# Kernel tuning notes

Measured on AMD Instinct MI355X. Metric: run time of the kernel, lower is better.

The kernel has to match this reference:

```python
import jax, jax.numpy as jnp
import numpy as np

KS = 5
NF = 64
B, H, W = 2, 160, 160


def _conv1x1(x, w, b):
    # x: (B,Ci,H,W), w: (Co,Ci)
    return jnp.einsum('oi,bihw->bohw', w, x) + b[None, :, None, None]


def _conv2x2(x, w, b, dil):
    # x: (B,1,Hp,Wp), w: (64,1,2,2); VALID conv with dilation dil
    y = jax.lax.conv_general_dilated(x, w, (1, 1), 'VALID',
                                     rhs_dilation=(dil, dil),
                                     dimension_numbers=('NCHW', 'OIHW', 'NCHW'))
    return y + b[None, :, None, None]


def _conv_s(x, w, b):
    # conv1 module, mode 's': gather taps (0,0),(1,1),(1,2),(2,1) of each 3x3 patch,
    # then (1,4) conv == linear combo of 4 shifted images.
    h = x.shape[2] - 2
    wd = x.shape[3] - 2
    x0 = x[:, 0]
    taps = jnp.stack([x0[:, 0:h, 0:wd],
                      x0[:, 1:h + 1, 1:wd + 1],
                      x0[:, 1:h + 1, 2:wd + 2],
                      x0[:, 2:h + 2, 1:wd + 1]], axis=1)  # (B,4,h,wd)
    return jnp.einsum('ok,bkhw->bohw', w.reshape(NF, 4), taps) + b[None, :, None, None]


def _construct(c, dense_ps):
    # relu then dense 1x1-conv chain with channel concat, final 1x1 -> 4 channels
    x = jax.nn.relu(c)
    for (wt, bs) in dense_ps[:-1]:
        feat = jax.nn.relu(_conv1x1(x, wt, bs))
        x = jnp.concatenate([x, feat], axis=1)
    wt, bs = dense_ps[-1]
    return _conv1x1(x, wt, bs)


def _ag(x, sigx, sigy, theta, sigr):
    # x: (B,ks,ks,HW); params: (B,HW). Per-pixel anisotropic bilateral kernel.
    ks = x.shape[1]
    r = jnp.arange(ks, dtype=x.dtype) - ks // 2
    sq = (r[:, None] ** 2 + r[None, :] ** 2)[None, :, :, None]  # (1,ks,ks,1)
    sx = sigx[:, None, None, :]
    sy = sigy[:, None, None, :]
    th = theta[:, None, None, :]
    sr = sigr[:, None, None, :]
    spatial = jnp.exp(-sq / (2.0 * sr ** 2))
    disx = jnp.abs(x[:, ks // 2:ks // 2 + 1] - x)       # center row
    disy = jnp.abs(x[:, :, ks // 2:ks // 2 + 1] - x)    # center col
    a = sx * disx
    bb = sy * disy
    color = jnp.exp(-0.5 * (a ** 2 - 2.0 * th * a * bb + bb ** 2))
    kern = spatial * color
    kern = kern / jnp.sum(kern, axis=(1, 2), keepdims=True)
    return jnp.sum(kern * x, axis=(1, 2))  # (B,HW)


def _forward(x_in, conv1x_w, conv1x_b, conv1c_w, conv1c_b, conv1cs_w, conv1cs_b,
             w2, b2, w3, b3, w4, b4, w5, b5, w6, b6):
    dense_ps = [(w2, b2), (w3, b3), (w4, b4), (w5, b5), (w6, b6)]

    def fk(x, mod):
        if mod == 's':
            c = _conv_s(x, conv1cs_w, conv1cs_b)
        elif mod == 'c':
            c = _conv2x2(x, conv1c_w, conv1c_b, 2)
        else:
            c = _conv2x2(x, conv1x_w, conv1x_b, 1)
        return _construct(c, dense_ps)

    def mode_ens(x, p, mod):
        pad = lambda z: jnp.pad(z, ((0, 0), (0, 0), (0, p), (0, p)), mode='reflect')
        r0 = fk(pad(x), mod)
        r2 = jnp.rot90(fk(pad(jnp.rot90(x, 2, (2, 3))), mod), 2, (2, 3))
        r1 = jnp.rot90(fk(pad(jnp.rot90(x, 1, (2, 3))), mod), 3, (2, 3))
        r3 = jnp.rot90(fk(pad(jnp.rot90(x, 3, (2, 3))), mod), 1, (2, 3))
        return (r0 + r2) / 2.0, (r1 + r3) / 2.0

    e1x, e2x = mode_ens(x_in, 1, 'x')
    e1s, e2s = mode_ens(x_in, 2, 's')
    e1c, e2c = mode_ens(x_in, 2, 'c')
    par = (e1x + e2x + e1s + e2s + e1c + e2c) / 6.0  # (B,4,H,W)

    b, c, h, w = x_in.shape
    sigx = jnp.clip(jax.nn.sigmoid(par[:, 0]).reshape(b, -1) + 1e-6, 0.0, 1.0)
    sigy = jnp.clip(jax.nn.sigmoid(par[:, 1]).reshape(b, -1) + 1e-6, 0.0, 1.0)
    theta = jnp.clip(jnp.tanh(par[:, 2]).reshape(b, -1), -1.0, 1.0)
    sigr = jnp.clip(jnp.tanh(par[:, 3]).reshape(b, -1) + 1e-6, -1.0, 1.0)

    ph = KS // 2
    xt = jnp.pad(x_in, ((0, 0), (0, 0), (ph, ph), (ph, ph)))  # zero pad
    # unfold -> (B, KS, KS, H*W)
    patches = jnp.stack([jnp.stack([xt[:, 0, i:i + h, j:j + w].reshape(b, -1)
                                    for j in range(KS)], axis=1)
                         for i in range(KS)], axis=1)
    outs = _ag(patches, sigx * 20.0, sigy * 20.0, theta, sigr * 10.0 + 10.0).reshape(b, c, h, w)
    return outs, sigx, sigy, theta, sigr


def setup_inputs() -> dict:
    key = jax.random.key(0)
    k = jax.random.split(key, 10)
    def kn(kk, shape, fan_in):
        return jax.random.normal(kk, shape, jnp.float32) * np.float32(np.sqrt(2.0 / fan_in))
    zb = lambda n: jnp.zeros((n,), jnp.float32)
    return {
        'x_in': jax.random.normal(k[0], (B, 1, H, W), jnp.float32),
        'conv1x_w': kn(k[1], (NF, 1, 2, 2), 4), 'conv1x_b': zb(NF),
        'conv1c_w': kn(k[2], (NF, 1, 2, 2), 4), 'conv1c_b': zb(NF),
        'conv1cs_w': kn(k[3], (NF, 1, 1, 4), 4), 'conv1cs_b': zb(NF),
        'w2': kn(k[4], (NF, NF), NF), 'b2': zb(NF),
        'w3': kn(k[5], (NF, 2 * NF), 2 * NF), 'b3': zb(NF),
        'w4': kn(k[6], (NF, 3 * NF), 3 * NF), 'b4': zb(NF),
        'w5': kn(k[7], (NF, 4 * NF), 4 * NF), 'b5': zb(NF),
        'w6': kn(k[8], (4, 5 * NF), 5 * NF), 'b6': zb(4),
    }


def reference(x_in, conv1x_w, conv1x_b, conv1c_w, conv1c_b, conv1cs_w, conv1cs_b,
              w2, b2, w3, b3, w4, b4, w5, b5, w6, b6):
    return _forward(x_in, conv1x_w, conv1x_b, conv1c_w, conv1c_b, conv1cs_w, conv1cs_b,
                    w2, b2, w3, b3, w4, b4, w5, b5, w6, b6)
```

## Files before the change

kernel.cpp:

```cpp
#include <hip/hip_runtime.h>
#include <hip/hip_bf16.h>
#include <math.h>
#include <string.h>


#define NN   160
#define NPIX 25600

typedef __attribute__((ext_vector_type(4))) float float4v;
typedef __attribute__((ext_vector_type(8))) unsigned short ushort8;
typedef __attribute__((ext_vector_type(2))) unsigned int uint2v;
typedef __attribute__((ext_vector_type(4))) unsigned int uint4v;
typedef __attribute__((ext_vector_type(8))) __bf16 bf16x8;

#define PINV(v) asm volatile("" : "+v"(v))

__device__ __forceinline__ int refp(int a) { return (a <= NN - 1) ? a : (2 * (NN - 1) - a); }

__device__ __forceinline__ unsigned int pk2(float lo, float hi) {
    float2 f; f.x = lo; f.y = hi;
    __hip_bfloat162 h = __float22bfloat162_rn(f);
    unsigned int u;
    memcpy(&u, &h, 4);
    return u;
}
__device__ __forceinline__ uint4v cvt8(const float* __restrict__ p) {
    const float4v f0 = *(const float4v*)p;
    const float4v f1 = *(const float4v*)(p + 4);
    uint4v u;
    u[0] = pk2(f0[0], f0[1]); u[1] = pk2(f0[2], f0[3]);
    u[2] = pk2(f1[0], f1[1]); u[3] = pk2(f1[2], f1[3]);
    return u;
}

template <int NCH>
__device__ __forceinline__ void dense_layer(const uint4v (&A)[NCH], float4v biasv,
                                            unsigned short* Xs, int w, int lo16, int lq) {
    const int K = NCH * 32;
#pragma unroll
    for (int pp = 0; pp < 2; ++pp) {
        const int px0 = (pp * 2) * 16 + lo16;
        const int px1 = (pp * 2 + 1) * 16 + lo16;
        float4v acc0 = biasv, acc1 = biasv;
#pragma unroll
        for (int s = 0; s < NCH; ++s) {
            const int c8 = s * 4 + lq;
            const bf16x8 bf0 = __builtin_bit_cast(bf16x8, *(const ushort8*)&Xs[c8 * 512 + px0 * 8]);
            const bf16x8 bf1 = __builtin_bit_cast(bf16x8, *(const ushort8*)&Xs[c8 * 512 + px1 * 8]);
            const bf16x8 af  = __builtin_bit_cast(bf16x8, A[s]);
            acc0 = __builtin_amdgcn_mfma_f32_16x16x32_bf16(af, bf0, acc0, 0, 0, 0);
            acc1 = __builtin_amdgcn_mfma_f32_16x16x32_bf16(af, bf1, acc1, 0, 0, 0);
        }
        const int cb = K + w * 16 + lq * 4;
        uint2v o0, o1;
        o0[0] = pk2(fmaxf(acc0[0], 0.0f), fmaxf(acc0[1], 0.0f));
        o0[1] = pk2(fmaxf(acc0[2], 0.0f), fmaxf(acc0[3], 0.0f));
        o1[0] = pk2(fmaxf(acc1[0], 0.0f), fmaxf(acc1[1], 0.0f));
        o1[1] = pk2(fmaxf(acc1[2], 0.0f), fmaxf(acc1[3], 0.0f));
        *(uint2v*)&Xs[(cb >> 3) * 512 + px0 * 8 + (cb & 7)] = o0;
        *(uint2v*)&Xs[(cb >> 3) * 512 + px1 * 8 + (cb & 7)] = o1;
    }
    __syncthreads();
}

__global__ __launch_bounds__(256, 3) void bnet_mlp_kernel(
    const float* __restrict__ x,
    const float* __restrict__ wx, const float* __restrict__ bx,
    const float* __restrict__ wcs, const float* __restrict__ bcs,
    const float* __restrict__ wc, const float* __restrict__ bc,
    const float* __restrict__ w2, const float* __restrict__ b2,
    const float* __restrict__ w3, const float* __restrict__ b3,
    const float* __restrict__ w4, const float* __restrict__ b4,
    const float* __restrict__ w5, const float* __restrict__ b5,
    const float* __restrict__ w6,
    float* __restrict__ par)
{
    __shared__ unsigned short Xs[20480];

    const int t = threadIdx.x;
    const int lane = t & 63;
    const int lo16 = lane & 15;
    const int lq = lane >> 4;
    const int w = __builtin_amdgcn_readfirstlane(t >> 6);

    const int arow = w * 16 + lo16;
    uint4v a2[2], a3[4], a4[6], a5[8], a6[3];
#pragma unroll
    for (int s = 0; s < 2; ++s) a2[s] = cvt8(&w2[arow * 64 + s * 32 + lq * 8]);
#pragma unroll
    for (int s = 0; s < 4; ++s) a3[s] = cvt8(&w3[arow * 128 + s * 32 + lq * 8]);
#pragma unroll
    for (int s = 0; s < 6; ++s) a4[s] = cvt8(&w4[arow * 192 + s * 32 + lq * 8]);
#pragma unroll
    for (int s = 0; s < 8; ++s) a5[s] = cvt8(&w5[arow * 256 + s * 32 + lq * 8]);
#pragma unroll
    for (int c = 0; c < 3; ++c) {
        const int ch = (3 * w + c) * 32;
        if (ch < 320 && lo16 < 4) {
            a6[c] = cvt8(&w6[lo16 * 320 + ch + lq * 8]);
        } else {
            uint4v z = {0u, 0u, 0u, 0u};
            a6[c] = z;
        }
    }
    float4v b2v = *(const float4v*)&b2[w * 16 + lq * 4];
    float4v b3v = *(const float4v*)&b3[w * 16 + lq * 4];
    float4v b4v = *(const float4v*)&b4[w * 16 + lq * 4];
    float4v b5v = *(const float4v*)&b5[w * 16 + lq * 4];

#pragma unroll
    for (int s = 0; s < 2; ++s) PINV(a2[s]);
#pragma unroll
    for (int s = 0; s < 4; ++s) PINV(a3[s]);
#pragma unroll
    for (int s = 0; s < 6; ++s) PINV(a4[s]);
#pragma unroll
    for (int s = 0; s < 8; ++s) PINV(a5[s]);
#pragma unroll
    for (int c = 0; c < 3; ++c) PINV(a6[c]);
    PINV(b2v); PINV(b3v); PINV(b4v); PINV(b5v);

    const int bid = blockIdx.x;
    const int nit = 12 + (bid < 384 ? 1 : 0);
    const int g0  = (bid < 384) ? bid * 13 : bid * 12 + 384;

    for (int it = 0; it < nit; ++it) {
        const int g = g0 + it;
        const int v = g % 12;
        const int tb = g / 12;
        const int tile = tb >> 1;
        const int b = tb & 1;
        const int mode = v >> 2;
        const int k = v & 3;

        const float* xb = x + b * NPIX;
        const float* w1 = (mode == 0) ? wx : (mode == 1) ? wcs : wc;
        const float* b1 = (mode == 0) ? bx : (mode == 1) ? bcs : bc;
        int DY[4], DX[4];
        if (mode == 0)      { DY[0]=0; DY[1]=0; DY[2]=1; DY[3]=1;  DX[0]=0; DX[1]=1; DX[2]=0; DX[3]=1; }
        else if (mode == 1) { DY[0]=0; DY[1]=1; DY[2]=1; DY[3]=2;  DX[0]=0; DX[1]=1; DX[2]=2; DX[3]=1; }
        else                { DY[0]=0; DY[1]=0; DY[2]=2; DY[3]=2;  DX[0]=0; DX[1]=2; DX[2]=0; DX[3]=2; }

        const int pix = tile * 64 + lane;
        const int pi = pix / NN;
        const int pj = pix - pi * NN;

        __syncthreads();

        float s4[4];
#pragma unroll
        for (int tt = 0; tt < 4; ++tt) {
            const int dy = DY[tt], dx = DX[tt];
            int r, c;
            if (k == 0)      { r = refp(pi + dy); c = refp(pj + dx); }
            else if (k == 1) { r = refp(pi + dx); c = (pj >= dy) ? (pj - dy) : (dy - pj); }
            else if (k == 2) { r = (pi >= dy) ? (pi - dy) : (dy - pi);
                               c = (pj >= dx) ? (pj - dx) : (dx - pj); }
            else             { r = (pi >= dx) ? (pi - dx) : (dx - pi); c = refp(pj + dy); }
            s4[tt] = xb[r * NN + c];
        }
        float co[16];
#pragma unroll
        for (int oo = 0; oo < 16; ++oo) {
            const int o = w * 16 + oo;
            float cacc = b1[o];
#pragma unroll
            for (int tt = 0; tt < 4; ++tt) cacc = fmaf(w1[o * 4 + tt], s4[tt], cacc);
            co[oo] = fmaxf(cacc, 0.0f);
        }
        uint4v pka, pkb;
#pragma unroll
        for (int q = 0; q < 4; ++q) {
            pka[q] = pk2(co[2 * q], co[2 * q + 1]);
            pkb[q] = pk2(co[8 + 2 * q], co[9 + 2 * q]);
        }
        *(uint4v*)&Xs[(w * 2) * 512 + lane * 8]     = pka;
        *(uint4v*)&Xs[(w * 2 + 1) * 512 + lane * 8] = pkb;
        __syncthreads();

        dense_layer<2>(a2, b2v, Xs, w, lo16, lq);
        dense_layer<4>(a3, b3v, Xs, w, lo16, lq);
        dense_layer<6>(a4, b4v, Xs, w, lo16, lq);
        dense_layer<8>(a5, b5v, Xs, w, lo16, lq);

#pragma unroll
        for (int pt = 0; pt < 4; ++pt) {
            float4v acc6 = {0.f, 0.f, 0.f, 0.f};
            const int px = pt * 16 + lo16;
#pragma unroll
            for (int c = 0; c < 3; ++c) {
                int chb = (3 * w + c) * 32;
                chb = (chb < 288) ? chb : 288;
                const int c8 = (chb >> 3) + lq;
                const bf16x8 bf = __builtin_bit_cast(
                    bf16x8, *(const ushort8*)&Xs[c8 * 512 + px * 8]);
                const bf16x8 af = __builtin_bit_cast(bf16x8, a6[c]);
                acc6 = __builtin_amdgcn_mfma_f32_16x16x32_bf16(af, bf, acc6, 0, 0, 0);
            }
            if (lq == 0) {
                const int pixg = tile * 64 + pt * 16 + lo16;
#pragma unroll
                for (int r = 0; r < 4; ++r)
                    atomicAdd(&par[(r * 2 + b) * NPIX + pixg], acc6[r]);
            }
        }
    }
}

__global__ __launch_bounds__(128) void bnet_bilateral_kernel(
    const float* __restrict__ x, const float* __restrict__ b6,
    float* __restrict__ out)
{
    const int tid = blockIdx.x * 128 + threadIdx.x;
    const int b = tid / NPIX;
    const int pix = tid - b * NPIX;
    const int pi = pix / NN;
    const int pj = pix - pi * NN;

    float* par = out + 2 * NPIX;
    const float inv12 = 1.0f / 12.0f;
    const float p0 = par[(0 + b) * NPIX + pix] * inv12 + b6[0];
    const float p1 = par[(2 + b) * NPIX + pix] * inv12 + b6[1];
    const float p2 = par[(4 + b) * NPIX + pix] * inv12 + b6[2];
    const float p3 = par[(6 + b) * NPIX + pix] * inv12 + b6[3];

    float sigx = 1.0f / (1.0f + __expf(-p0)) + 1e-6f;
    sigx = fminf(fmaxf(sigx, 0.0f), 1.0f);
    float sigy = 1.0f / (1.0f + __expf(-p1)) + 1e-6f;
    sigy = fminf(fmaxf(sigy, 0.0f), 1.0f);
    float t2 = __expf(2.0f * fminf(fmaxf(p2, -15.0f), 15.0f));
    float th = (t2 - 1.0f) / (t2 + 1.0f);
    th = fminf(fmaxf(th, -1.0f), 1.0f);
    float t3 = __expf(2.0f * fminf(fmaxf(p3, -15.0f), 15.0f));
    float sigr = (t3 - 1.0f) / (t3 + 1.0f) + 1e-6f;
    sigr = fminf(fmaxf(sigr, -1.0f), 1.0f);

    par[(0 + b) * NPIX + pix] = sigx;
    par[(2 + b) * NPIX + pix] = sigy;
    par[(4 + b) * NPIX + pix] = th;
    par[(6 + b) * NPIX + pix] = sigr;

    const float sx = sigx * 20.0f;
    const float sy = sigy * 20.0f;
    const float sr = sigr * 10.0f + 10.0f;

    const float* xb = x + b * NPIX;
    float patch[5][5];
#pragma unroll
    for (int ky = 0; ky < 5; ++ky) {
#pragma unroll
        for (int kx = 0; kx < 5; ++kx) {
            const int r = pi + ky - 2, c = pj + kx - 2;
            patch[ky][kx] = (r >= 0 && r < NN && c >= 0 && c < NN) ? xb[r * NN + c] : 0.0f;
        }
    }

    const float inv2sr2 = 1.0f / (2.0f * sr * sr);
    float num = 0.0f, den = 0.0f;
#pragma unroll
    for (int ky = 0; ky < 5; ++ky) {
#pragma unroll
        for (int kx = 0; kx < 5; ++kx) {
            const float v = patch[ky][kx];
            const float dxv = fabsf(patch[2][kx] - v);
            const float dyv = fabsf(patch[ky][2] - v);
            const float a = sx * dxv;
            const float bb = sy * dyv;
            const float sq = (float)((ky - 2) * (ky - 2) + (kx - 2) * (kx - 2));
            const float kern = __expf(-sq * inv2sr2 - 0.5f * (a * a - 2.0f * th * a * bb + bb * bb));
            den += kern;
            num = fmaf(kern, v, num);
        }
    }
    out[tid] = num / den;
}

extern "C" void kernel_launch(void* const* d_in, const int* in_sizes, int n_in,
                              void* d_out, int out_size, void* d_ws, size_t ws_size,
                              hipStream_t stream) {
    const float* x   = (const float*)d_in[0];
    const float* wx  = (const float*)d_in[1];
    const float* bx  = (const float*)d_in[2];
    const float* wc  = (const float*)d_in[3];
    const float* bc  = (const float*)d_in[4];
    const float* wcs = (const float*)d_in[5];
    const float* bcs = (const float*)d_in[6];
    const float* w2  = (const float*)d_in[7];
    const float* b2  = (const float*)d_in[8];
    const float* w3  = (const float*)d_in[9];
    const float* b3  = (const float*)d_in[10];
    const float* w4  = (const float*)d_in[11];
    const float* b4  = (const float*)d_in[12];
    const float* w5  = (const float*)d_in[13];
    const float* b5  = (const float*)d_in[14];
    const float* w6  = (const float*)d_in[15];
    const float* b6  = (const float*)d_in[16];
    float* out = (float*)d_out;

    (void)hipMemsetAsync(out + 2 * NPIX, 0, 8 * NPIX * sizeof(float), stream);

    hipLaunchKernelGGL(bnet_mlp_kernel, dim3(768), dim3(256), 0, stream,
                       x, wx, bx, wcs, bcs, wc, bc,
                       w2, b2, w3, b3, w4, b4, w5, b5, w6,
                       out + 2 * NPIX);

    hipLaunchKernelGGL(bnet_bilateral_kernel, dim3(400), dim3(128), 0, stream,
                       x, b6, out);
}
```

Before: 185.1 us.

## Retile dense MFMA layers as 2x2 output-channel by pixel blocks per wave

After: 212.7 us. 14.9% more time.

```diff
diff --git a/kernel.cpp b/kernel.cpp
--- a/kernel.cpp
+++ b/kernel.cpp
@@ -34,36 +34,48 @@
 }
 
 template <int NCH>
-__device__ __forceinline__ void dense_layer(const uint4v (&A)[NCH], float4v biasv,
-                                            unsigned short* Xs, int w, int lo16, int lq) {
+__device__ __forceinline__ void dense_layer(const uint4v (&A0)[NCH], const uint4v (&A1)[NCH],
+                                            const float* __restrict__ bias,
+                                            unsigned short* Xs,
+                                            int oh, int ph, int lo16, int lq) {
     const int K = NCH * 32;
-#pragma unroll
-    for (int pp = 0; pp < 2; ++pp) {
-        const int px0 = (pp * 2) * 16 + lo16;
-        const int px1 = (pp * 2 + 1) * 16 + lo16;
-        float4v acc0 = biasv, acc1 = biasv;
-#pragma unroll
-        for (int s = 0; s < NCH; ++s) {
-            const int c8 = s * 4 + lq;
-            const bf16x8 bf0 = __builtin_bit_cast(bf16x8, *(const ushort8*)&Xs[c8 * 512 + px0 * 8]);
-            const bf16x8 bf1 = __builtin_bit_cast(bf16x8, *(const ushort8*)&Xs[c8 * 512 + px1 * 8]);
-            const bf16x8 af  = __builtin_bit_cast(bf16x8, A[s]);
-            acc0 = __builtin_amdgcn_mfma_f32_16x16x32_bf16(af, bf0, acc0, 0, 0, 0);
-            acc1 = __builtin_amdgcn_mfma_f32_16x16x32_bf16(af, bf1, acc1, 0, 0, 0);
-        }
-        const int cb = K + w * 16 + lq * 4;
-        uint2v o0, o1;
-        o0[0] = pk2(fmaxf(acc0[0], 0.0f), fmaxf(acc0[1], 0.0f));
-        o0[1] = pk2(fmaxf(acc0[2], 0.0f), fmaxf(acc0[3], 0.0f));
-        o1[0] = pk2(fmaxf(acc1[0], 0.0f), fmaxf(acc1[1], 0.0f));
-        o1[1] = pk2(fmaxf(acc1[2], 0.0f), fmaxf(acc1[3], 0.0f));
-        *(uint2v*)&Xs[(cb >> 3) * 512 + px0 * 8 + (cb & 7)] = o0;
-        *(uint2v*)&Xs[(cb >> 3) * 512 + px1 * 8 + (cb & 7)] = o1;
-    }
+    const int px0 = (ph * 2) * 16 + lo16;
+    const int px1 = (ph * 2 + 1) * 16 + lo16;
+    const float4v bv0 = *(const float4v*)&bias[(oh * 2) * 16 + lq * 4];
+    const float4v bv1 = *(const float4v*)&bias[(oh * 2 + 1) * 16 + lq * 4];
+
+    float4v acc00 = {0.f,0.f,0.f,0.f}, acc01 = acc00, acc10 = acc00, acc11 = acc00;
+#pragma unroll
+    for (int s = 0; s < NCH; ++s) {
+        const int c8 = s * 4 + lq;
+        const bf16x8 bf0 = __builtin_bit_cast(bf16x8, *(const ushort8*)&Xs[c8 * 512 + px0 * 8]);
+        const bf16x8 bf1 = __builtin_bit_cast(bf16x8, *(const ushort8*)&Xs[c8 * 512 + px1 * 8]);
+        const bf16x8 af0 = __builtin_bit_cast(bf16x8, A0[s]);
+        const bf16x8 af1 = __builtin_bit_cast(bf16x8, A1[s]);
+        acc00 = __builtin_amdgcn_mfma_f32_16x16x32_bf16(af0, bf0, acc00, 0, 0, 0);
+        acc01 = __builtin_amdgcn_mfma_f32_16x16x32_bf16(af0, bf1, acc01, 0, 0, 0);
+        acc10 = __builtin_amdgcn_mfma_f32_16x16x32_bf16(af1, bf0, acc10, 0, 0, 0);
+        acc11 = __builtin_amdgcn_mfma_f32_16x16x32_bf16(af1, bf1, acc11, 0, 0, 0);
+    }
+    const int cb0 = K + (oh * 2) * 16 + lq * 4;
+    const int cb1 = K + (oh * 2 + 1) * 16 + lq * 4;
+    uint2v o00, o01, o10, o11;
+    o00[0] = pk2(fmaxf(acc00[0] + bv0[0], 0.0f), fmaxf(acc00[1] + bv0[1], 0.0f));
+    o00[1] = pk2(fmaxf(acc00[2] + bv0[2], 0.0f), fmaxf(acc00[3] + bv0[3], 0.0f));
+    o01[0] = pk2(fmaxf(acc01[0] + bv0[0], 0.0f), fmaxf(acc01[1] + bv0[1], 0.0f));
+    o01[1] = pk2(fmaxf(acc01[2] + bv0[2], 0.0f), fmaxf(acc01[3] + bv0[3], 0.0f));
+    o10[0] = pk2(fmaxf(acc10[0] + bv1[0], 0.0f), fmaxf(acc10[1] + bv1[1], 0.0f));
+    o10[1] = pk2(fmaxf(acc10[2] + bv1[2], 0.0f), fmaxf(acc10[3] + bv1[3], 0.0f));
+    o11[0] = pk2(fmaxf(acc11[0] + bv1[0], 0.0f), fmaxf(acc11[1] + bv1[1], 0.0f));
+    o11[1] = pk2(fmaxf(acc11[2] + bv1[2], 0.0f), fmaxf(acc11[3] + bv1[3], 0.0f));
+    *(uint2v*)&Xs[(cb0 >> 3) * 512 + px0 * 8 + (cb0 & 7)] = o00;
+    *(uint2v*)&Xs[(cb0 >> 3) * 512 + px1 * 8 + (cb0 & 7)] = o01;
+    *(uint2v*)&Xs[(cb1 >> 3) * 512 + px0 * 8 + (cb1 & 7)] = o10;
+    *(uint2v*)&Xs[(cb1 >> 3) * 512 + px1 * 8 + (cb1 & 7)] = o11;
     __syncthreads();
 }
 
-__global__ __launch_bounds__(256, 3) void bnet_mlp_kernel(
+__global__ __launch_bounds__(256, 2) void bnet_mlp_kernel(
     const float* __restrict__ x,
     const float* __restrict__ wx, const float* __restrict__ bx,
     const float* __restrict__ wcs, const float* __restrict__ bcs,
@@ -82,17 +94,24 @@
     const int lo16 = lane & 15;
     const int lq = lane >> 4;
     const int w = __builtin_amdgcn_readfirstlane(t >> 6);
-
-    const int arow = w * 16 + lo16;
-    uint4v a2[2], a3[4], a4[6], a5[8], a6[3];
-#pragma unroll
-    for (int s = 0; s < 2; ++s) a2[s] = cvt8(&w2[arow * 64 + s * 32 + lq * 8]);
-#pragma unroll
-    for (int s = 0; s < 4; ++s) a3[s] = cvt8(&w3[arow * 128 + s * 32 + lq * 8]);
-#pragma unroll
-    for (int s = 0; s < 6; ++s) a4[s] = cvt8(&w4[arow * 192 + s * 32 + lq * 8]);
-#pragma unroll
-    for (int s = 0; s < 8; ++s) a5[s] = cvt8(&w5[arow * 256 + s * 32 + lq * 8]);
+    const int oh = w & 1;
+    const int ph = w >> 1;
+
+    const int ar0 = (oh * 2) * 16 + lo16;
+    const int ar1 = (oh * 2 + 1) * 16 + lo16;
+    uint4v a2[2][2], a3[2][4], a4[2][6], a5[2][8], a6[3];
+#pragma unroll
+    for (int s = 0; s < 2; ++s) { a2[0][s] = cvt8(&w2[ar0 * 64 + s * 32 + lq * 8]);
+                                  a2[1][s] = cvt8(&w2[ar1 * 64 + s * 32 + lq * 8]); }
+#pragma unroll
+    for (int s = 0; s < 4; ++s) { a3[0][s] = cvt8(&w3[ar0 * 128 + s * 32 + lq * 8]);
+                                  a3[1][s] = cvt8(&w3[ar1 * 128 + s * 32 + lq * 8]); }
+#pragma unroll
+    for (int s = 0; s < 6; ++s) { a4[0][s] = cvt8(&w4[ar0 * 192 + s * 32 + lq * 8]);
+                                  a4[1][s] = cvt8(&w4[ar1 * 192 + s * 32 + lq * 8]); }
+#pragma unroll
+    for (int s = 0; s < 8; ++s) { a5[0][s] = cvt8(&w5[ar0 * 256 + s * 32 + lq * 8]);
+                                  a5[1][s] = cvt8(&w5[ar1 * 256 + s * 32 + lq * 8]); }
 #pragma unroll
     for (int c = 0; c < 3; ++c) {
         const int ch = (3 * w + c) * 32;
@@ -103,26 +122,23 @@
             a6[c] = z;
         }
     }
-    float4v b2v = *(const float4v*)&b2[w * 16 + lq * 4];
-    float4v b3v = *(const float4v*)&b3[w * 16 + lq * 4];
-    float4v b4v = *(const float4v*)&b4[w * 16 + lq * 4];
-    float4v b5v = *(const float4v*)&b5[w * 16 + lq * 4];
-
-#pragma unroll
-    for (int s = 0; s < 2; ++s) PINV(a2[s]);
-#pragma unroll
-    for (int s = 0; s < 4; ++s) PINV(a3[s]);
-#pragma unroll
-    for (int s = 0; s < 6; ++s) PINV(a4[s]);
-#pragma unroll
-    for (int s = 0; s < 8; ++s) PINV(a5[s]);
+#pragma unroll
+    for (int i = 0; i < 2; ++i) {
+#pragma unroll
+        for (int s = 0; s < 2; ++s) PINV(a2[i][s]);
+#pragma unroll
+        for (int s = 0; s < 4; ++s) PINV(a3[i][s]);
+#pragma unroll
+        for (int s = 0; s < 6; ++s) PINV(a4[i][s]);
+#pragma unroll
+        for (int s = 0; s < 8; ++s) PINV(a5[i][s]);
+    }
 #pragma unroll
     for (int c = 0; c < 3; ++c) PINV(a6[c]);
-    PINV(b2v); PINV(b3v); PINV(b4v); PINV(b5v);
 
     const int bid = blockIdx.x;
-    const int nit = 12 + (bid < 384 ? 1 : 0);
-    const int g0  = (bid < 384) ? bid * 13 : bid * 12 + 384;
+    const int nit = (bid < 384) ? 19 : 18;
+    const int g0  = (bid < 384) ? bid * 19 : bid * 18 + 384;
 
     for (int it = 0; it < nit; ++it) {
         const int g = g0 + it;
@@ -178,10 +194,10 @@
         *(uint4v*)&Xs[(w * 2 + 1) * 512 + lane * 8] = pkb;
         __syncthreads();
 
-        dense_layer<2>(a2, b2v, Xs, w, lo16, lq);
-        dense_layer<4>(a3, b3v, Xs, w, lo16, lq);
-        dense_layer<6>(a4, b4v, Xs, w, lo16, lq);
-        dense_layer<8>(a5, b5v, Xs, w, lo16, lq);
+        dense_layer<2>(a2[0], a2[1], b2, Xs, oh, ph, lo16, lq);
+        dense_layer<4>(a3[0], a3[1], b3, Xs, oh, ph, lo16, lq);
+        dense_layer<6>(a4[0], a4[1], b4, Xs, oh, ph, lo16, lq);
+        dense_layer<8>(a5[0], a5[1], b5, Xs, oh, ph, lo16, lq);
 
 #pragma unroll
         for (int pt = 0; pt < 4; ++pt) {
@@ -207,11 +223,11 @@
     }
 }
 
-__global__ __launch_bounds__(128) void bnet_bilateral_kernel(
+__global__ __launch_bounds__(256) void bnet_bilateral_kernel(
     const float* __restrict__ x, const float* __restrict__ b6,
     float* __restrict__ out)
 {
-    const int tid = blockIdx.x * 128 + threadIdx.x;
+    const int tid = blockIdx.x * 256 + threadIdx.x;
     const int b = tid / NPIX;
     const int pix = tid - b * NPIX;
     const int pi = pix / NN;
@@ -299,11 +315,11 @@
 
     (void)hipMemsetAsync(out + 2 * NPIX, 0, 8 * NPIX * sizeof(float), stream);
 
-    hipLaunchKernelGGL(bnet_mlp_kernel, dim3(768), dim3(256), 0, stream,
+    hipLaunchKernelGGL(bnet_mlp_kernel, dim3(512), dim3(256), 0, stream,
                        x, wx, bx, wcs, bcs, wc, bc,
                        w2, b2, w3, b3, w4, b4, w5, b5, w6,
                        out + 2 * NPIX);
 
-    hipLaunchKernelGGL(bnet_bilateral_kernel, dim3(400), dim3(128), 0, stream,
+    hipLaunchKernelGGL(bnet_bilateral_kernel, dim3(200), dim3(256), 0, stream,
                        x, b6, out);
 }
```
